# Kernel optimization log

Hardware: AMD Instinct MI355X
Metric: run time of the kernel (lower is better)

## Reference

```python
import jax, jax.numpy as jnp
import numpy as np

EMBED = 2048
N_HEAD = 32
N_KV = 8
HEAD_DIM = 64
GROUP = N_HEAD // N_KV


def _rope_tables(seq_len, head_dim):
    inv_freq = 1.0 / (10000.0 ** (jnp.arange(0, head_dim, 2, dtype=jnp.float32) / head_dim))
    ang = jnp.arange(seq_len, dtype=jnp.float32)[:, None] * inv_freq[None, :]  # [S, D/2]
    ang = jnp.concatenate([ang, ang], axis=-1)  # [S, D]
    return jnp.cos(ang), jnp.sin(ang)


def apply_rope(x, cos, sin, offset=0):
    # x: [B, H, S, D]
    S, D = x.shape[2], x.shape[3]
    x1, x2 = x[..., : D // 2], x[..., D // 2 :]
    c = cos[offset : offset + S][None, None]
    s = sin[offset : offset + S][None, None]
    rotated = jnp.concatenate([-x2, x1], axis=-1)
    return (x * c + rotated * s).astype(x.dtype)


def setup_inputs() -> dict:
    key = jax.random.key(0)
    kx, kq, kk, kv, ko = jax.random.split(key, 5)
    B, S = 2, 2048
    x = jax.random.normal(kx, (B, S, EMBED), dtype=jnp.float32)
    mask = jnp.triu(jnp.ones((S, S), dtype=bool), k=1)  # causal: True = masked
    cos, sin = _rope_tables(S, HEAD_DIM)
    std = 0.02
    Wq = jax.random.normal(kq, (EMBED, EMBED), dtype=jnp.float32) * std
    Wk = jax.random.normal(kk, (EMBED, N_KV * HEAD_DIM), dtype=jnp.float32) * std
    Wv = jax.random.normal(kv, (EMBED, N_KV * HEAD_DIM), dtype=jnp.float32) * std
    Wo = jax.random.normal(ko, (EMBED, EMBED), dtype=jnp.float32) * std
    return {"x": x, "mask": mask, "cos": cos, "sin": sin,
            "Wq": Wq, "Wk": Wk, "Wv": Wv, "Wo": Wo}


def reference(x, mask, cos, sin, Wq, Wk, Wv, Wo):
    B, S, E = x.shape
    # projections (no bias)
    q = (x @ Wq).reshape(B, S, N_HEAD, HEAD_DIM).transpose(0, 2, 1, 3)  # [B,H,S,D]
    k = (x @ Wk).reshape(B, S, N_KV, HEAD_DIM).transpose(0, 2, 1, 3)    # [B,G,S,D]
    v = (x @ Wv).reshape(B, S, N_KV, HEAD_DIM).transpose(0, 2, 1, 3)    # [B,G,S,D]
    q = apply_rope(q, cos, sin, offset=0)
    k = apply_rope(k, cos, sin, offset=0)
    next_k, next_v = k, v  # kv cache to return
    # GQA: head h uses kv group h // GROUP; avoid repeat_interleave via reshape
    qg = q.reshape(B, N_KV, GROUP, S, HEAD_DIM)
    scores = jnp.einsum('bgjsd,bgtd->bgjst', qg, k) / np.float32(np.sqrt(HEAD_DIM))
    scores = jnp.where(mask[None, None, None], -jnp.inf, scores)
    attn = jax.nn.softmax(scores, axis=-1)
    out = jnp.einsum('bgjst,bgtd->bgjsd', attn, v)          # [B,G,group,S,D]
    out = out.reshape(B, N_HEAD, S, HEAD_DIM).transpose(0, 2, 1, 3).reshape(B, S, E)
    return out @ Wo, next_k, next_v
```

## Files before the change

kernel.cpp:

```cpp
#include <hip/hip_runtime.h>
#include <hip/hip_bf16.h>
#include <math.h>

#define NH 32
#define NKV 8
#define HD 64
#define B_ 2
#define S_ 2048
#define E_ 2048
#define M_ 4096

typedef unsigned short ushort_t;
typedef __attribute__((ext_vector_type(8))) short short8;
typedef __attribute__((ext_vector_type(4))) short short4v;
typedef __attribute__((ext_vector_type(4))) float floatx4;

__device__ inline unsigned short f2bf(float f) {
  unsigned int u = __float_as_uint(f);
  return (unsigned short)((u + 0x7FFFu + ((u >> 16) & 1u)) >> 16);
}

__device__ inline float fexp2(float x) {
  float r;
  asm("v_exp_f32 %0, %1" : "=v"(r) : "v"(x));
  return r;
}

__device__ inline void ld_lds16(const void* g, void* l) {
  __builtin_amdgcn_global_load_lds((__attribute__((address_space(1))) void*)g,
                                   (__attribute__((address_space(3))) void*)l, 16, 0, 0);
}

__device__ inline void transp32(const float* __restrict__ in, ushort_t* __restrict__ out,
                                int R, int C, int bx, int by, int tid, float (*tile)[33]) {
  int c0 = bx * 32, r0 = by * 32;
  int x = tid & 31, y0 = tid >> 5;
  for (int i = 0; i < 4; i++) {
    int r = y0 + i * 8;
    tile[r][x] = in[(size_t)(r0 + r) * C + c0 + x];
  }
  __syncthreads();
  for (int i = 0; i < 4; i++) {
    int r = y0 + i * 8;
    out[(size_t)(c0 + r) * R + r0 + x] = f2bf(tile[x][r]);
  }
}

__global__ __launch_bounds__(256) void prep(const float* __restrict__ x,
                                            ushort_t* __restrict__ xb,
                                            const float* __restrict__ Wq,
                                            const float* __restrict__ Wk,
                                            const float* __restrict__ Wv,
                                            const float* __restrict__ Wo,
                                            ushort_t* __restrict__ WT,
                                            ushort_t* __restrict__ WoT) {
  __shared__ float tile[32][33];
  int bid = blockIdx.x, tid = threadIdx.x;
  if (bid < 4096) {
    size_t i = ((size_t)bid * 256 + tid) * 8;
    float4 a = *(const float4*)(x + i);
    float4 b = *(const float4*)(x + i + 4);
    short8 o;
    o[0] = (short)f2bf(a.x); o[1] = (short)f2bf(a.y);
    o[2] = (short)f2bf(a.z); o[3] = (short)f2bf(a.w);
    o[4] = (short)f2bf(b.x); o[5] = (short)f2bf(b.y);
    o[6] = (short)f2bf(b.z); o[7] = (short)f2bf(b.w);
    *(short8*)(xb + i) = o;
    return;
  }
  bid -= 4096;
  if (bid < 4096) { transp32(Wq, WT, 2048, 2048, bid & 63, bid >> 6, tid, tile); return; }
  bid -= 4096;
  if (bid < 1024) { transp32(Wk, WT + 2048 * 2048, 2048, 512, bid & 15, bid >> 4, tid, tile); return; }
  bid -= 1024;
  if (bid < 1024) { transp32(Wv, WT + 2560 * 2048, 2048, 512, bid & 15, bid >> 4, tid, tile); return; }
  bid -= 1024;
  transp32(Wo, WoT, 2048, 2048, bid & 63, bid >> 6, tid, tile);
}

__global__ __launch_bounds__(256) void transpose_v(const float* __restrict__ outv,
                                                   ushort_t* __restrict__ vt) {
  __shared__ float t64[64][65];
  int bg = blockIdx.y;
  int tt = blockIdx.x;
  int s0 = tt * 64;
  int tid = threadIdx.x;
  size_t ibase = (size_t)bg * S_ * HD + (size_t)s0 * HD;
  for (int i = tid; i < 1024; i += 256) {
    int sr = i >> 4, dc = (i & 15) * 4;
    float4 v = *(const float4*)(outv + ibase + (size_t)sr * HD + dc);
    t64[sr][dc] = v.x; t64[sr][dc + 1] = v.y; t64[sr][dc + 2] = v.z; t64[sr][dc + 3] = v.w;
  }
  __syncthreads();
  size_t obase = ((size_t)bg * 32 + tt) * 4096;
  for (int i = tid; i < 512; i += 256) {
    int d = i >> 3, ss = (i & 7) * 8;
    short8 o;
#pragma unroll
    for (int e = 0; e < 8; e++) o[e] = (short)f2bf(t64[ss + e][d]);
    *(short8*)(vt + obase + d * 64 + (ss ^ ((d & 7) << 3))) = o;
  }
}

__device__ __forceinline__ void gemm128_core(const ushort_t* __restrict__ Ag,
                                             const ushort_t* __restrict__ Bg,
                                             floatx4 (&acc)[4][4]) {
  __shared__ __align__(16) ushort_t As[2][128][64];
  __shared__ __align__(16) ushort_t Bs[2][128][64];
  int tid = threadIdx.x;
  int w = tid >> 6, lane = tid & 63;
  int wm = (w >> 1) * 64, wn = (w & 1) * 64;
  int lr = lane & 15, quad = lane >> 4;
  int sx = lr & 7;
  char* Asb = (char*)As;
  char* Bsb = (char*)Bs;

  size_t so[4];
#pragma unroll
  for (int s = 0; s < 4; s++)
    so[s] = (size_t)(w * 32 + s * 8 + (lane >> 3)) * 4096 + (size_t)(((lane & 7) ^ (lane >> 3)) * 16);
  const char* abase = (const char*)Ag;
  const char* bbase = (const char*)Bg;

#define STAGE128(buf, kt)                                          \
  do {                                                             \
    size_t ko = (size_t)(kt) * 128;                                \
    char* Ad = Asb + (buf) * 16384 + w * 4096;                     \
    char* Bd = Bsb + (buf) * 16384 + w * 4096;                     \
    _Pragma("unroll") for (int s = 0; s < 4; s++) {                \
      ld_lds16(abase + so[s] + ko, Ad + s * 1024);                 \
      ld_lds16(bbase + so[s] + ko, Bd + s * 1024);                 \
    }                                                              \
  } while (0)

  STAGE128(0, 0);
  __syncthreads();

  int cur = 0;
  for (int kt = 0; kt < 32; kt++) {
    if (kt < 31) STAGE128(cur ^ 1, kt + 1);
    const char* Ab = Asb + cur * 16384;
    const char* Bb = Bsb + cur * 16384;
    short8 af[4][2], bfr[4][2];
#pragma unroll
    for (int i = 0; i < 4; i++) {
      size_t rb = (size_t)(wm + i * 16 + lr) * 128;
#pragma unroll
      for (int ks = 0; ks < 2; ks++)
        af[i][ks] = *(const short8*)(Ab + rb + (((ks * 4 + quad) ^ sx) << 4));
    }
#pragma unroll
    for (int j = 0; j < 4; j++) {
      size_t rb = (size_t)(wn + j * 16 + lr) * 128;
#pragma unroll
      for (int ks = 0; ks < 2; ks++)
        bfr[j][ks] = *(const short8*)(Bb + rb + (((ks * 4 + quad) ^ sx) << 4));
    }
#pragma unroll
    for (int i = 0; i < 4; i++)
#pragma unroll
      for (int j = 0; j < 4; j++) {
        acc[i][j] = __builtin_amdgcn_mfma_f32_16x16x32_bf16(af[i][0], bfr[j][0], acc[i][j], 0, 0, 0);
        acc[i][j] = __builtin_amdgcn_mfma_f32_16x16x32_bf16(af[i][1], bfr[j][1], acc[i][j], 0, 0, 0);
      }
    __syncthreads();
    cur ^= 1;
  }
#undef STAGE128
}

__global__ __launch_bounds__(256) void gemm_qkv(const ushort_t* __restrict__ xb,
                                                const ushort_t* __restrict__ WT,
                                                ushort_t* __restrict__ qbf,
                                                float* __restrict__ outk,
                                                ushort_t* __restrict__ kbf,
                                                float* __restrict__ outv,
                                                const float* __restrict__ cosP,
                                                const float* __restrict__ sinP) {
  int o = blockIdx.y * 24 + blockIdx.x;
  int xcd = o & 7, i = o >> 3;
  int mg = xcd >> 1, ng = xcd & 1;
  int m0 = (mg * 8 + i / 12) * 128;
  int n0 = (ng * 12 + i % 12) * 128;
  int tid = threadIdx.x;
  int w = tid >> 6, lane = tid & 63;
  int wm = (w >> 1) * 64, wn = (w & 1) * 64;
  int lr = lane & 15, quad = lane >> 4;

  floatx4 acc[4][4] = {};
  gemm128_core(xb + (size_t)m0 * 2048, WT + (size_t)n0 * 2048, acc);

  if (n0 < 2048) {
    const float QS = 0.125f * 1.4426950408889634f;
#pragma unroll
    for (int i2 = 0; i2 < 4; i2++)
#pragma unroll
      for (int j = 0; j < 2; j++) {
        int d = j * 16 + lr;
#pragma unroll
        for (int r = 0; r < 4; r++) {
          int row = m0 + wm + i2 * 16 + quad * 4 + r;
          int s = row & (S_ - 1);
          float c = cosP[s * 64 + d], sn = sinP[s * 64 + d];
          float x1 = acc[i2][j][r], x2 = acc[i2][j + 2][r];
          size_t oo = (size_t)row * 2048 + n0 + wn + d;
          qbf[oo] = f2bf((x1 * c - x2 * sn) * QS);
          qbf[oo + 32] = f2bf((x2 * c + x1 * sn) * QS);
        }
      }
  } else if (n0 < 2560) {
    int h = (n0 - 2048 + wn) >> 6;
#pragma unroll
    for (int i2 = 0; i2 < 4; i2++)
#pragma unroll
      for (int j = 0; j < 2; j++) {
        int d = j * 16 + lr;
#pragma unroll
        for (int r = 0; r < 4; r++) {
          int row = m0 + wm + i2 * 16 + quad * 4 + r;
          int s = row & (S_ - 1), b = row >> 11;
          float c = cosP[s * 64 + d], sn = sinP[s * 64 + d];
          float x1 = acc[i2][j][r], x2 = acc[i2][j + 2][r];
          float y1 = x1 * c - x2 * sn, y2 = x2 * c + x1 * sn;
          size_t rowb = ((size_t)(b * NKV + h) * S_ + s) * 64;
          int xr = (s & 7) << 3;
          outk[rowb + d] = y1; outk[rowb + d + 32] = y2;
          kbf[rowb + (d ^ xr)] = f2bf(y1);
          kbf[rowb + ((d + 32) ^ xr)] = f2bf(y2);
        }
      }
  } else {
    int h = (n0 - 2560 + wn) >> 6;
#pragma unroll
    for (int i2 = 0; i2 < 4; i2++)
#pragma unroll
      for (int j = 0; j < 4; j++) {
        int d = j * 16 + lr;
#pragma unroll
        for (int r = 0; r < 4; r++) {
          int row = m0 + wm + i2 * 16 + quad * 4 + r;
          int s = row & (S_ - 1), b = row >> 11;
          outv[((size_t)(b * NKV + h) * S_ + s) * 64 + d] = acc[i2][j][r];
        }
      }
  }
}

__global__ __launch_bounds__(256) void gemm_o(const ushort_t* __restrict__ ctx,
                                              const ushort_t* __restrict__ WoT,
                                              float* __restrict__ y) {
  int o = blockIdx.y * 16 + blockIdx.x;
  int xcd = o & 7, i = o >> 3;
  int mg = xcd >> 1, ng = xcd & 1;
  int m0 = (mg * 8 + (i >> 3)) * 128;
  int n0 = (ng * 8 + (i & 7)) * 128;
  int tid = threadIdx.x;
  int w = tid >> 6, lane = tid & 63;
  int wm = (w >> 1) * 64, wn = (w & 1) * 64;
  int lr = lane & 15, quad = lane >> 4;

  floatx4 acc[4][4] = {};
  gemm128_core(ctx + (size_t)m0 * 2048, WoT + (size_t)n0 * 2048, acc);

#pragma unroll
  for (int i2 = 0; i2 < 4; i2++)
#pragma unroll
    for (int j = 0; j < 4; j++) {
      int row = m0 + wm + i2 * 16 + quad * 4;
      int col = n0 + wn + j * 16 + lr;
#pragma unroll
      for (int r = 0; r < 4; r++)
        y[(size_t)(row + r) * 2048 + col] = acc[i2][j][r];
    }
}

__global__ __launch_bounds__(256, 4) void attn2(ushort_t* __restrict__ q,
                                                const ushort_t* __restrict__ k,
                                                const ushort_t* __restrict__ vt) {
  __shared__ __align__(16) ushort_t KV[2][2][64][64];
  __shared__ __align__(16) ushort_t Ps[4][16][64];
  int bh = blockIdx.x;
  int qt = 31 - blockIdx.y;
  int b = bh >> 5, h = bh & 31, g = h >> 2;
  int tid = threadIdx.x;
  int w = tid >> 6, lane = tid & 63;
  int lr = lane & 15, quad = lane >> 4;

  int qg = qt * 64 + w * 16 + lr;
  short8 aq0, aq1;
  {
    const ushort_t* qp = q + ((size_t)(b * S_ + qg) * NH + h) * HD;
    aq0 = *(const short8*)(qp + quad * 8);
    aq1 = *(const short8*)(qp + 32 + quad * 8);
  }
  floatx4 od[4] = {};
  float mi = -INFINITY, li = 0.f;

  const char* ksrc = (const char*)(k + (size_t)(b * NKV + g) * S_ * HD) + w * 2048 + lane * 16;
  const char* vsrc = (const char*)(vt + (size_t)(b * NKV + g) * S_ * HD) + w * 2048 + lane * 16;
  char* dB = (char*)&KV[0][0][0][0] + w * 2048;

  int sw = (lr & 7) << 4;
  int ro0 = (quad * 16) ^ sw;
  int ro1 = (64 + quad * 16) ^ sw;
  char* Pw = (char*)&Ps[0][0][0] + w * 2048;

  ld_lds16(ksrc, dB);
  ld_lds16(ksrc + 1024, dB + 1024);
  ld_lds16(vsrc, dB + 8192);
  ld_lds16(vsrc + 1024, dB + 8192 + 1024);
  asm volatile("s_waitcnt vmcnt(0)" ::: "memory");
  __syncthreads();

  int cur = 0;
  for (int t = 0; t <= qt; t++) {
    if (t < qt) {
      const char* kn = ksrc + (size_t)(t + 1) * 8192;
      const char* vn = vsrc + (size_t)(t + 1) * 8192;
      char* d = dB + (cur ^ 1) * 16384;
      ld_lds16(kn, d); ld_lds16(kn + 1024, d + 1024);
      ld_lds16(vn, d + 8192); ld_lds16(vn + 1024, d + 8192 + 1024);
    }
    const char* Kb = (const char*)&KV[cur][0][0][0];
    const char* Vb = (const char*)&KV[cur][1][0][0];
    floatx4 sc[4];
    __builtin_amdgcn_s_setprio(1);
#pragma unroll
    for (int kn = 0; kn < 4; kn++) {
      short8 a0 = *(const short8*)(Kb + (kn * 16 + lr) * 128 + ro0);
      short8 a1 = *(const short8*)(Kb + (kn * 16 + lr) * 128 + ro1);
      floatx4 c = {};
      c = __builtin_amdgcn_mfma_f32_16x16x32_bf16(a0, aq0, c, 0, 0, 0);
      c = __builtin_amdgcn_mfma_f32_16x16x32_bf16(a1, aq1, c, 0, 0, 0);
      sc[kn] = c;
    }
    __builtin_amdgcn_s_setprio(0);
    float pv[16];
#pragma unroll
    for (int kn = 0; kn < 4; kn++)
#pragma unroll
      for (int r = 0; r < 4; r++) pv[kn * 4 + r] = sc[kn][r];
    if (t == qt) {
#pragma unroll
      for (int e = 0; e < 16; e++) {
        int kg = t * 64 + (e >> 2) * 16 + quad * 4 + (e & 3);
        if (kg > qg) pv[e] = -INFINITY;
      }
    }
    float mx = pv[0];
#pragma unroll
    for (int e = 1; e < 16; e++) mx = fmaxf(mx, pv[e]);
    mx = fmaxf(mx, __shfl_xor(mx, 16));
    mx = fmaxf(mx, __shfl_xor(mx, 32));
    if (__any(mx > mi + 11.5f)) {
      float mn = fmaxf(mi, mx);
      float al = fexp2(mi - mn);
      li *= al;
#pragma unroll
      for (int dn = 0; dn < 4; dn++) {
        od[dn][0] *= al; od[dn][1] *= al; od[dn][2] *= al; od[dn][3] *= al;
      }
      mi = mn;
    }
    float ps = 0.f;
#pragma unroll
    for (int e = 0; e < 16; e++) {
      pv[e] = fexp2(pv[e] - mi);
      ps += pv[e];
    }
    ps += __shfl_xor(ps, 16);
    ps += __shfl_xor(ps, 32);
    li += ps;
#pragma unroll
    for (int kn = 0; kn < 4; kn++) {
      unsigned int u0, u1;
      asm("v_cvt_pk_bf16_f32 %0, %1, %2" : "=v"(u0) : "v"(pv[kn * 4 + 0]), "v"(pv[kn * 4 + 1]));
      asm("v_cvt_pk_bf16_f32 %0, %1, %2" : "=v"(u1) : "v"(pv[kn * 4 + 2]), "v"(pv[kn * 4 + 3]));
      uint2 uu; uu.x = u0; uu.y = u1;
      *(uint2*)(Pw + lr * 128 + ((kn * 32 + quad * 8) ^ sw)) = uu;
    }
    short8 pb0 = *(const short8*)(Pw + lr * 128 + ro0);
    short8 pb1 = *(const short8*)(Pw + lr * 128 + ro1);
    __builtin_amdgcn_s_setprio(1);
#pragma unroll
    for (int dn = 0; dn < 4; dn++) {
      short8 va = *(const short8*)(Vb + (dn * 16 + lr) * 128 + ro0);
      short8 vb = *(const short8*)(Vb + (dn * 16 + lr) * 128 + ro1);
      od[dn] = __builtin_amdgcn_mfma_f32_16x16x32_bf16(va, pb0, od[dn], 0, 0, 0);
      od[dn] = __builtin_amdgcn_mfma_f32_16x16x32_bf16(vb, pb1, od[dn], 0, 0, 0);
    }
    __builtin_amdgcn_s_setprio(0);
    asm volatile("s_waitcnt vmcnt(0)" ::: "memory");
    __syncthreads();
    cur ^= 1;
  }
  float inv = 1.f / li;
  ushort_t* outp = q + ((size_t)(b * S_ + qg) * NH + h) * HD;
#pragma unroll
  for (int dn = 0; dn < 4; dn++) {
    short4v u;
    u[0] = (short)f2bf(od[dn][0] * inv); u[1] = (short)f2bf(od[dn][1] * inv);
    u[2] = (short)f2bf(od[dn][2] * inv); u[3] = (short)f2bf(od[dn][3] * inv);
    *(short4v*)(outp + dn * 16 + quad * 4) = u;
  }
}

extern "C" void kernel_launch(void* const* d_in, const int* in_sizes, int n_in,
                              void* d_out, int out_size, void* d_ws, size_t ws_size,
                              hipStream_t stream) {
  const float* x = (const float*)d_in[0];
  const float* cosT = (const float*)d_in[2];
  const float* sinT = (const float*)d_in[3];
  const float* Wq = (const float*)d_in[4];
  const float* Wk = (const float*)d_in[5];
  const float* Wv = (const float*)d_in[6];
  const float* Wo = (const float*)d_in[7];

  char* ws = (char*)d_ws;
  ushort_t* WT = (ushort_t*)(ws);
  ushort_t* WoT = (ushort_t*)(ws + 12582912);
  ushort_t* xb = (ushort_t*)(ws + 20971520);
  ushort_t* qbf = (ushort_t*)(ws + 37748736);
  ushort_t* kbf = (ushort_t*)(ws + 54525952);
  ushort_t* vt = (ushort_t*)(ws + 58720256);

  float* y = (float*)d_out;
  float* outk = y + (size_t)M_ * E_;
  float* outv = outk + (size_t)B_ * NKV * S_ * HD;

  prep<<<dim3(14336), 256, 0, stream>>>(x, xb, Wq, Wk, Wv, Wo, WT, WoT);

  gemm_qkv<<<dim3(24, 32), 256, 0, stream>>>(xb, WT, qbf, outk, kbf, outv, cosT, sinT);
  transpose_v<<<dim3(32, 16), 256, 0, stream>>>(outv, vt);

  attn2<<<dim3(64, 32), 256, 0, stream>>>(qbf, kbf, vt);

  gemm_o<<<dim3(16, 32), 256, 0, stream>>>(qbf, WoT, y);
}
```

Baseline: 322.2 us.

## Rewrite QKV GEMM as 256x256 8-wave tiles and fuse V transpose into epilogue

The QKV projection GEMM moves from 128x128 tiles with 4 waves to 256x256 tiles with 8 waves (192 blocks). It uses a four-phase pipelined schedule with direct global-to-LDS loads, explicit vmcnt waits and barriers, and s_setprio around the MFMA clusters. The epilogue now also writes the swizzled bf16 transposed V directly, which removes the separate transpose_v kernel launch and its re-read of outv. Only 192 blocks may underfill the CUs, and the larger tile raises register and LDS pressure.

```diff
diff --git a/kernel.cpp b/kernel.cpp
--- a/kernel.cpp
+++ b/kernel.cpp
@@ -78,27 +78,155 @@
   transp32(Wo, WoT, 2048, 2048, bid & 63, bid >> 6, tid, tile);
 }
 
-__global__ __launch_bounds__(256) void transpose_v(const float* __restrict__ outv,
-                                                   ushort_t* __restrict__ vt) {
-  __shared__ float t64[64][65];
-  int bg = blockIdx.y;
-  int tt = blockIdx.x;
-  int s0 = tt * 64;
+__global__ __launch_bounds__(512) void gemm_qkv(const ushort_t* __restrict__ xb,
+                                                const ushort_t* __restrict__ WT,
+                                                ushort_t* __restrict__ qbf,
+                                                float* __restrict__ outk,
+                                                ushort_t* __restrict__ kbf,
+                                                float* __restrict__ outv,
+                                                ushort_t* __restrict__ vt,
+                                                const float* __restrict__ cosP,
+                                                const float* __restrict__ sinP) {
+  __shared__ __align__(16) ushort_t L8[2][2][2][128][64];
+  char* Lb = (char*)L8;
+  int bid = blockIdx.x;
+  int xcd = bid & 7, ii = bid >> 3;
+  int mg = xcd >> 1, ng = xcd & 1;
+  int m0 = (mg * 4 + ii / 6) * 256;
+  int n0 = (ng * 6 + ii % 6) * 256;
   int tid = threadIdx.x;
-  size_t ibase = (size_t)bg * S_ * HD + (size_t)s0 * HD;
-  for (int i = tid; i < 1024; i += 256) {
-    int sr = i >> 4, dc = (i & 15) * 4;
-    float4 v = *(const float4*)(outv + ibase + (size_t)sr * HD + dc);
-    t64[sr][dc] = v.x; t64[sr][dc + 1] = v.y; t64[sr][dc + 2] = v.z; t64[sr][dc + 3] = v.w;
-  }
-  __syncthreads();
-  size_t obase = ((size_t)bg * 32 + tt) * 4096;
-  for (int i = tid; i < 512; i += 256) {
-    int d = i >> 3, ss = (i & 7) * 8;
-    short8 o;
-#pragma unroll
-    for (int e = 0; e < 8; e++) o[e] = (short)f2bf(t64[ss + e][d]);
-    *(short8*)(vt + obase + d * 64 + (ss ^ ((d & 7) << 3))) = o;
+  int w8 = tid >> 6, lane = tid & 63;
+  int wrq = w8 >> 1, wcq = w8 & 1;
+  int lr = lane & 15, quad = lane >> 4;
+  int sx = lr & 7;
+  int srow = w8 * 16 + (lane >> 3);
+  int schunk = (lane & 7) ^ (lane >> 3);
+  const char* abase = (const char*)(xb + (size_t)m0 * 2048);
+  const char* bbase = (const char*)(WT + (size_t)n0 * 2048);
+  floatx4 acc[4][2][4] = {};
+
+#define STG(T, U)                                                                        \
+  do {                                                                                   \
+    const int mat_ = (U)&1, half_ = (U) >> 1;                                            \
+    const char* sp = (mat_ ? bbase : abase) + (size_t)(half_ * 128 + srow) * 4096 +      \
+                     (size_t)(T)*128 + schunk * 16;                                      \
+    char* dp = Lb + (((T)&1) * 65536) + mat_ * 32768 + half_ * 16384 + w8 * 2048;        \
+    ld_lds16(sp, dp);                                                                    \
+    ld_lds16(sp + (size_t)8 * 4096, dp + 1024);                                          \
+  } while (0)
+
+#define PH(T, P, MH_, NH_, WAITS, DOSTAGE)                                               \
+  do {                                                                                   \
+    asm volatile(WAITS ::: "memory");                                                    \
+    const char* Ab_ = Lb + (((T)&1) * 65536) + (MH_)*16384;                              \
+    const char* Bb_ = Lb + (((T)&1) * 65536) + 32768 + (NH_)*16384;                      \
+    short8 af_[2][2], bf_[4][2];                                                         \
+    _Pragma("unroll") for (int i = 0; i < 2; i++) {                                      \
+      size_t rb = (size_t)(wrq * 32 + i * 16 + lr) * 128;                                \
+      _Pragma("unroll") for (int ks = 0; ks < 2; ks++)                                   \
+          af_[i][ks] = *(const short8*)(Ab_ + rb + (((ks * 4 + quad) ^ sx) << 4));       \
+    }                                                                                    \
+    _Pragma("unroll") for (int j = 0; j < 4; j++) {                                      \
+      size_t rb = (size_t)(wcq * 64 + j * 16 + lr) * 128;                                \
+      _Pragma("unroll") for (int ks = 0; ks < 2; ks++)                                   \
+          bf_[j][ks] = *(const short8*)(Bb_ + rb + (((ks * 4 + quad) ^ sx) << 4));       \
+    }                                                                                    \
+    if (DOSTAGE) STG((T) + 1, P);                                                        \
+    __builtin_amdgcn_s_setprio(1);                                                       \
+    _Pragma("unroll") for (int i = 0; i < 2; i++) _Pragma("unroll") for (int j = 0;      \
+                                                                         j < 4; j++) {  \
+      acc[P][i][j] =                                                                     \
+          __builtin_amdgcn_mfma_f32_16x16x32_bf16(af_[i][0], bf_[j][0], acc[P][i][j],    \
+                                                  0, 0, 0);                              \
+      acc[P][i][j] =                                                                     \
+          __builtin_amdgcn_mfma_f32_16x16x32_bf16(af_[i][1], bf_[j][1], acc[P][i][j],    \
+                                                  0, 0, 0);                              \
+    }                                                                                    \
+    __builtin_amdgcn_s_setprio(0);                                                       \
+  } while (0)
+
+  STG(0, 0); STG(0, 1); STG(0, 2); STG(0, 3);
+
+  for (int kt = 0; kt < 31; kt++) {
+    PH(kt, 0, 0, 0, "s_waitcnt vmcnt(4)\n\ts_barrier", 1);
+    PH(kt, 1, 1, 0, "s_waitcnt vmcnt(4)\n\ts_barrier", 1);
+    PH(kt, 2, 1, 1, "s_waitcnt vmcnt(4)\n\ts_barrier", 1);
+    PH(kt, 3, 0, 1, "s_barrier", 1);
+  }
+  PH(31, 0, 0, 0, "s_waitcnt vmcnt(4)\n\ts_barrier", 0);
+  PH(31, 1, 1, 0, "s_waitcnt vmcnt(2)\n\ts_barrier", 0);
+  PH(31, 2, 1, 1, "s_waitcnt vmcnt(0)\n\ts_barrier", 0);
+  PH(31, 3, 0, 1, "s_barrier", 0);
+#undef STG
+#undef PH
+
+  const int MHs[4] = {0, 1, 1, 0}, NHs[4] = {0, 0, 1, 1};
+  if (n0 < 2048) {
+    const float QS = 0.125f * 1.4426950408889634f;
+#pragma unroll
+    for (int p = 0; p < 4; p++)
+#pragma unroll
+      for (int i = 0; i < 2; i++)
+#pragma unroll
+        for (int j = 0; j < 2; j++) {
+          int d = j * 16 + lr;
+#pragma unroll
+          for (int r = 0; r < 4; r++) {
+            int row = m0 + MHs[p] * 128 + wrq * 32 + i * 16 + quad * 4 + r;
+            int s = row & (S_ - 1);
+            float c = cosP[s * 64 + d], sn = sinP[s * 64 + d];
+            float x1 = acc[p][i][j][r], x2 = acc[p][i][j + 2][r];
+            size_t oo = (size_t)row * 2048 + n0 + NHs[p] * 128 + wcq * 64 + d;
+            qbf[oo] = f2bf((x1 * c - x2 * sn) * QS);
+            qbf[oo + 32] = f2bf((x2 * c + x1 * sn) * QS);
+          }
+        }
+  } else if (n0 < 2560) {
+#pragma unroll
+    for (int p = 0; p < 4; p++) {
+      int h = ((n0 - 2048) >> 6) + NHs[p] * 2 + wcq;
+#pragma unroll
+      for (int i = 0; i < 2; i++)
+#pragma unroll
+        for (int j = 0; j < 2; j++) {
+          int d = j * 16 + lr;
+#pragma unroll
+          for (int r = 0; r < 4; r++) {
+            int row = m0 + MHs[p] * 128 + wrq * 32 + i * 16 + quad * 4 + r;
+            int s = row & (S_ - 1), b = row >> 11;
+            float c = cosP[s * 64 + d], sn = sinP[s * 64 + d];
+            float x1 = acc[p][i][j][r], x2 = acc[p][i][j + 2][r];
+            float y1 = x1 * c - x2 * sn, y2 = x2 * c + x1 * sn;
+            size_t rowb = ((size_t)(b * NKV + h) * S_ + s) * 64;
+            int xr = (s & 7) << 3;
+            outk[rowb + d] = y1; outk[rowb + d + 32] = y2;
+            kbf[rowb + (d ^ xr)] = f2bf(y1);
+            kbf[rowb + ((d + 32) ^ xr)] = f2bf(y2);
+          }
+        }
+    }
+  } else {
+#pragma unroll
+    for (int p = 0; p < 4; p++) {
+      int h = ((n0 - 2560) >> 6) + NHs[p] * 2 + wcq;
+#pragma unroll
+      for (int i = 0; i < 2; i++)
+#pragma unroll
+        for (int j = 0; j < 4; j++) {
+          int d = j * 16 + lr;
+          int row0 = m0 + MHs[p] * 128 + wrq * 32 + i * 16 + quad * 4;
+          int s0 = row0 & (S_ - 1), b = row0 >> 11;
+#pragma unroll
+          for (int r = 0; r < 4; r++)
+            outv[((size_t)(b * NKV + h) * S_ + s0 + r) * 64 + d] = acc[p][i][j][r];
+          int tt = s0 >> 6, s4 = s0 & 63;
+          short4v u;
+          u[0] = (short)f2bf(acc[p][i][j][0]); u[1] = (short)f2bf(acc[p][i][j][1]);
+          u[2] = (short)f2bf(acc[p][i][j][2]); u[3] = (short)f2bf(acc[p][i][j][3]);
+          *(short4v*)(vt + ((size_t)(b * NKV + h) * 32 + tt) * 4096 + d * 64 +
+                      (s4 ^ ((d & 7) << 3))) = u;
+        }
+    }
   }
 }
 
@@ -169,83 +297,6 @@
 #undef STAGE128
 }
 
-__global__ __launch_bounds__(256) void gemm_qkv(const ushort_t* __restrict__ xb,
-                                                const ushort_t* __restrict__ WT,
-                                                ushort_t* __restrict__ qbf,
-                                                float* __restrict__ outk,
-                                                ushort_t* __restrict__ kbf,
-                                                float* __restrict__ outv,
-                                                const float* __restrict__ cosP,
-                                                const float* __restrict__ sinP) {
-  int o = blockIdx.y * 24 + blockIdx.x;
-  int xcd = o & 7, i = o >> 3;
-  int mg = xcd >> 1, ng = xcd & 1;
-  int m0 = (mg * 8 + i / 12) * 128;
-  int n0 = (ng * 12 + i % 12) * 128;
-  int tid = threadIdx.x;
-  int w = tid >> 6, lane = tid & 63;
-  int wm = (w >> 1) * 64, wn = (w & 1) * 64;
-  int lr = lane & 15, quad = lane >> 4;
-
-  floatx4 acc[4][4] = {};
-  gemm128_core(xb + (size_t)m0 * 2048, WT + (size_t)n0 * 2048, acc);
-
-  if (n0 < 2048) {
-    const float QS = 0.125f * 1.4426950408889634f;
-#pragma unroll
-    for (int i2 = 0; i2 < 4; i2++)
-#pragma unroll
-      for (int j = 0; j < 2; j++) {
-        int d = j * 16 + lr;
-#pragma unroll
-        for (int r = 0; r < 4; r++) {
-          int row = m0 + wm + i2 * 16 + quad * 4 + r;
-          int s = row & (S_ - 1);
-          float c = cosP[s * 64 + d], sn = sinP[s * 64 + d];
-          float x1 = acc[i2][j][r], x2 = acc[i2][j + 2][r];
-          size_t oo = (size_t)row * 2048 + n0 + wn + d;
-          qbf[oo] = f2bf((x1 * c - x2 * sn) * QS);
-          qbf[oo + 32] = f2bf((x2 * c + x1 * sn) * QS);
-        }
-      }
-  } else if (n0 < 2560) {
-    int h = (n0 - 2048 + wn) >> 6;
-#pragma unroll
-    for (int i2 = 0; i2 < 4; i2++)
-#pragma unroll
-      for (int j = 0; j < 2; j++) {
-        int d = j * 16 + lr;
-#pragma unroll
-        for (int r = 0; r < 4; r++) {
-          int row = m0 + wm + i2 * 16 + quad * 4 + r;
-          int s = row & (S_ - 1), b = row >> 11;
-          float c = cosP[s * 64 + d], sn = sinP[s * 64 + d];
-          float x1 = acc[i2][j][r], x2 = acc[i2][j + 2][r];
-          float y1 = x1 * c - x2 * sn, y2 = x2 * c + x1 * sn;
-          size_t rowb = ((size_t)(b * NKV + h) * S_ + s) * 64;
-          int xr = (s & 7) << 3;
-          outk[rowb + d] = y1; outk[rowb + d + 32] = y2;
-          kbf[rowb + (d ^ xr)] = f2bf(y1);
-          kbf[rowb + ((d + 32) ^ xr)] = f2bf(y2);
-        }
-      }
-  } else {
-    int h = (n0 - 2560 + wn) >> 6;
-#pragma unroll
-    for (int i2 = 0; i2 < 4; i2++)
-#pragma unroll
-      for (int j = 0; j < 4; j++) {
-        int d = j * 16 + lr;
-#pragma unroll
-        for (int r = 0; r < 4; r++) {
-          int row = m0 + wm + i2 * 16 + quad * 4 + r;
-          int s = row & (S_ - 1), b = row >> 11;
-          outv[((size_t)(b * NKV + h) * S_ + s) * 64 + d] = acc[i2][j][r];
-        }
-      }
-  }
-}
-
 __global__ __launch_bounds__(256) void gemm_o(const ushort_t* __restrict__ ctx,
                                               const ushort_t* __restrict__ WoT,
                                               float* __restrict__ y) {
@@ -430,8 +481,7 @@
 
   prep<<<dim3(14336), 256, 0, stream>>>(x, xb, Wq, Wk, Wv, Wo, WT, WoT);
 
-  gemm_qkv<<<dim3(24, 32), 256, 0, stream>>>(xb, WT, qbf, outk, kbf, outv, cosT, sinT);
-  transpose_v<<<dim3(32, 16), 256, 0, stream>>>(outv, vt);
+  gemm_qkv<<<dim3(192), 512, 0, stream>>>(xb, WT, qbf, outk, kbf, outv, vt, cosT, sinT);
 
   attn2<<<dim3(64, 32), 256, 0, stream>>>(qbf, kbf, vt);
 
```

New measurement: 308.6 us. -4.2%, faster.
